# Optimization experiments

Measured on AMD Instinct MI355X. Metric: run time of the kernel, lower is better.

Reference implementation:

```python
import jax, jax.numpy as jnp
import numpy as np

N = 20000          # nodes
E = 320000         # directed edges (self-loops added in reference)
F_IN = 128         # input node features
HEADS = 8
HID = 64           # per-head hidden channels
G = 64             # graphs in the batch
NUM_CLASSES = 10
NEG_SLOPE = 0.2    # PyG GATConv LeakyReLU slope


def _gat_layer(x, src, dst, W, a_src, a_dst, bias, n_nodes):
    """PyG-style GATConv: messages flow src->dst, softmax over incoming edges."""
    H, C = a_src.shape
    h = (x @ W).reshape(n_nodes, H, C)                     # [N,H,C]
    asrc = jnp.einsum('nhc,hc->nh', h, a_src)              # [N,H]
    adst = jnp.einsum('nhc,hc->nh', h, a_dst)              # [N,H]
    e = jax.nn.leaky_relu(asrc[src] + adst[dst], NEG_SLOPE)  # [Etot,H]
    emax = jax.ops.segment_max(e, dst, num_segments=n_nodes)  # [N,H]
    ee = jnp.exp(e - emax[dst])
    denom = jax.ops.segment_sum(ee, dst, num_segments=n_nodes)
    alpha = ee / (denom[dst] + 1e-16)                      # [Etot,H]
    out = jax.ops.segment_sum(h[src] * alpha[:, :, None], dst, num_segments=n_nodes)
    return out.reshape(n_nodes, H * C) + bias


def setup_inputs() -> dict:
    key = jax.random.key(0)
    ks = jax.random.split(key, 10)
    x = jax.random.normal(ks[0], (N, F_IN), jnp.float32)
    edge_index = jax.random.randint(ks[1], (2, E), 0, N, jnp.int32)
    batch = jnp.sort(jax.random.randint(ks[2], (N,), 0, G, jnp.int32))
    # layer 1: F_IN -> HEADS*HID (concat)
    W1 = jax.random.normal(ks[3], (F_IN, HEADS * HID), jnp.float32) / np.float32(np.sqrt(F_IN))
    a_src1 = jax.random.normal(ks[4], (HEADS, HID), jnp.float32) / np.float32(np.sqrt(HID))
    a_dst1 = jax.random.normal(ks[5], (HEADS, HID), jnp.float32) / np.float32(np.sqrt(HID))
    b1 = jnp.zeros((HEADS * HID,), jnp.float32)
    # layer 2: HEADS*HID -> NUM_CLASSES (1 head)
    W2 = jax.random.normal(ks[6], (HEADS * HID, NUM_CLASSES), jnp.float32) / np.float32(np.sqrt(HEADS * HID))
    a_src2 = jax.random.normal(ks[7], (1, NUM_CLASSES), jnp.float32) / np.float32(np.sqrt(NUM_CLASSES))
    a_dst2 = jax.random.normal(ks[8], (1, NUM_CLASSES), jnp.float32) / np.float32(np.sqrt(NUM_CLASSES))
    b2 = jnp.zeros((NUM_CLASSES,), jnp.float32)
    return {"x": x, "edge_index": edge_index, "batch": batch,
            "W1": W1, "a_src1": a_src1, "a_dst1": a_dst1, "b1": b1,
            "W2": W2, "a_src2": a_src2, "a_dst2": a_dst2, "b2": b2}


def reference(x, edge_index, batch, W1, a_src1, a_dst1, b1, W2, a_src2, a_dst2, b2):
    n = x.shape[0]
    loop = jnp.arange(n, dtype=edge_index.dtype)   # add_self_loops=True (PyG default)
    src = jnp.concatenate([edge_index[0], loop])
    dst = jnp.concatenate([edge_index[1], loop])
    h = jax.nn.elu(_gat_layer(x, src, dst, W1, a_src1, a_dst1, b1, n))
    h = _gat_layer(h, src, dst, W2, a_src2, a_dst2, b2, n)
    # PowerMeanAggregation with default p=1.0 == mean pooling per graph
    sums = jax.ops.segment_sum(h, batch, num_segments=G)                    # [G,NC]
    counts = jax.ops.segment_sum(jnp.ones((n, 1), h.dtype), batch, num_segments=G)
    return sums / jnp.maximum(counts, 1.0)
```

## Files before the change

### kernel.cpp

```cpp
#include <hip/hip_runtime.h>
#include <hip/hip_bf16.h>

typedef unsigned short ushort_t;
typedef unsigned int uint_t;
typedef unsigned char uchar_t;

typedef __attribute__((ext_vector_type(8))) short bf16x8;
typedef __attribute__((ext_vector_type(4))) float f32x4;
typedef __attribute__((ext_vector_type(2))) float f32x2;

__device__ __forceinline__ float bf2f(ushort_t u) {
    union { uint_t i; float f; } v; v.i = ((uint_t)u) << 16; return v.f;
}
__device__ __forceinline__ ushort_t f2bf(float f) {
    __hip_bfloat16 h = __float2bfloat16(f);
    ushort_t u; __builtin_memcpy(&u, &h, 2); return u;
}
__device__ __forceinline__ uchar_t f2fp8(float v) {
    int p = __builtin_amdgcn_cvt_pk_fp8_f32(v, v, 0, false);
    return (uchar_t)(p & 0xff);
}
__device__ __forceinline__ float leaky(float v) { return (v > 0.f) ? v : 0.2f * v; }

#define PO_AS1 0
#define PO_AD1 512
#define PO_B1  1024
#define PO_W2  1536
#define PO_AS2 6656
#define PO_AD2 6666
#define PO_B2  6676
#define PTOT   6686

__device__ __forceinline__ bool detect_fp32_local(const ushort_t* __restrict__ xa) {
    __shared__ int cnt;
    if (threadIdx.x == 0) cnt = 0;
    __syncthreads();
    int bad = 0;
    for (int i = threadIdx.x; i < 4096; i += 256) {
        float v = bf2f(xa[i]);
        if (!(fabsf(v) < 1e4f)) bad++;
    }
    if (bad) atomicAdd(&cnt, bad);
    __syncthreads();
    return cnt >= 16;
}

__global__ __launch_bounds__(256) void k_prep(const void* __restrict__ x,
                                              const void* __restrict__ W1,
                                              const void* as1, const void* ad1,
                                              const void* b1, const void* W2,
                                              const void* as2, const void* ad2,
                                              const void* b2,
                                              ushort_t* __restrict__ W1t,
                                              float* __restrict__ prm,
                                              int* __restrict__ deg,
                                              float* __restrict__ gacc,
                                              int* __restrict__ flag, int N) {
    int b = blockIdx.x, t = threadIdx.x;
    if (b < 283) {
        bool isf = detect_fp32_local((const ushort_t*)x);
        if (b == 0 && t == 0) *flag = isf ? 1 : 0;
        if (b < 256) {
            int idx = b * 256 + t;
            int n = idx & 511, k = idx >> 9;
            float v = isf ? ((const float*)W1)[k * 512 + n]
                          : bf2f(((const ushort_t*)W1)[k * 512 + n]);
            W1t[n * 128 + k] = f2bf(v);
        } else {
            int i = (b - 256) * 256 + t;
            if (i < PTOT) {
                const void* src; int off;
                if (i < 512)       { src = as1; off = i; }
                else if (i < 1024) { src = ad1; off = i - 512; }
                else if (i < 1536) { src = b1;  off = i - 1024; }
                else if (i < 6656) { src = W2;  off = i - 1536; }
                else if (i < 6666) { src = as2; off = i - 6656; }
                else if (i < 6676) { src = ad2; off = i - 6666; }
                else               { src = b2;  off = i - 6676; }
                prm[i] = isf ? ((const float*)src)[off] : bf2f(((const ushort_t*)src)[off]);
            }
        }
    } else if (b < 362) {
        int i = (b - 283) * 256 + t;
        if (i < N) deg[i] = 0;
    } else {
        for (int i = t; i < 640; i += 256) gacc[i] = 0.f;
    }
}

__global__ __launch_bounds__(256) void k_gemm_hist(const void* __restrict__ xraw,
                                                   const ushort_t* __restrict__ w1t,
                                                   const float* __restrict__ prm,
                                                   const int* __restrict__ ei,
                                                   const int* __restrict__ flag,
                                                   uchar_t* __restrict__ h1,
                                                   float* __restrict__ asrcf,
                                                   float* __restrict__ adstf,
                                                   int* __restrict__ deg,
                                                   int E, int Etot) {
    int b = blockIdx.x, t = threadIdx.x;
    if (b >= 1250) {
        int e = (b - 1250) * 256 + t;
        if (e < Etot) {
            int dst = (e < E) ? ei[E + e] : (e - E);
            atomicAdd(&deg[dst], 1);
        }
        return;
    }
    int wave = t >> 6, lane = t & 63;
    int m0 = b * 16;
    bool isf = (*flag != 0);
    __shared__ ushort_t sA[16 * 128];
    {
        ushort_t tmp[8];
        if (isf) {
            const float4* x4 = (const float4*)((const float*)xraw + (size_t)m0 * 128);
            float4 f0 = x4[2 * t], f1 = x4[2 * t + 1];
            tmp[0] = f2bf(f0.x); tmp[1] = f2bf(f0.y); tmp[2] = f2bf(f0.z); tmp[3] = f2bf(f0.w);
            tmp[4] = f2bf(f1.x); tmp[5] = f2bf(f1.y); tmp[6] = f2bf(f1.z); tmp[7] = f2bf(f1.w);
        } else {
            const uint4* x4 = (const uint4*)((const ushort_t*)xraw + (size_t)m0 * 128);
            uint4 u = x4[t];
            __builtin_memcpy(tmp, &u, 16);
        }
        *reinterpret_cast<uint4*>(&sA[t * 8]) = *reinterpret_cast<uint4*>(tmp);
    }
    __syncthreads();
    int mr = lane & 15, quad = lane >> 4;
    int n0 = wave * 128;
    f32x4 acc[8];
#pragma unroll
    for (int ct = 0; ct < 8; ++ct) acc[ct] = {0.f, 0.f, 0.f, 0.f};
#pragma unroll
    for (int kk = 0; kk < 4; ++kk) {
        bf16x8 a = *reinterpret_cast<const bf16x8*>(&sA[mr * 128 + quad * 8 + kk * 32]);
#pragma unroll
        for (int ct = 0; ct < 8; ++ct) {
            bf16x8 bb = *reinterpret_cast<const bf16x8*>(
                &w1t[(size_t)(n0 + ct * 16 + mr) * 128 + quad * 8 + kk * 32]);
            acc[ct] = __builtin_amdgcn_mfma_f32_16x16x32_bf16(a, bb, acc[ct], 0, 0, 0);
        }
    }
    int col = lane & 15;
#pragma unroll
    for (int hh = 0; hh < 2; ++hh) {
        float ps[4] = {0.f, 0.f, 0.f, 0.f}, pd[4] = {0.f, 0.f, 0.f, 0.f};
#pragma unroll
        for (int c4 = 0; c4 < 4; ++c4) {
            int ct = hh * 4 + c4;
            int abscol = n0 + ct * 16 + col;
            float asv = prm[PO_AS1 + abscol];
            float adv = prm[PO_AD1 + abscol];
#pragma unroll
            for (int r = 0; r < 4; ++r) {
                h1[(size_t)(m0 + quad * 4 + r) * 512 + abscol] = f2fp8(acc[ct][r]);
                ps[r] += acc[ct][r] * asv;
                pd[r] += acc[ct][r] * adv;
            }
        }
#pragma unroll
        for (int off = 1; off <= 8; off <<= 1) {
#pragma unroll
            for (int r = 0; r < 4; ++r) {
                ps[r] += __shfl_xor(ps[r], off, 64);
                pd[r] += __shfl_xor(pd[r], off, 64);
            }
        }
        if (col == 0) {
            int head = 2 * wave + hh;
#pragma unroll
            for (int r = 0; r < 4; ++r) {
                asrcf[(m0 + quad * 4 + r) * 8 + head] = ps[r];
                adstf[(m0 + quad * 4 + r) * 8 + head] = pd[r];
            }
        }
    }
}

__global__ __launch_bounds__(256) void k_scan(const int* __restrict__ deg,
                                              int* __restrict__ rowptr,
                                              int* __restrict__ cursor, int N) {
    int b = blockIdx.x, t = threadIdx.x;
    int lane = t & 63, wv = t >> 6;
    __shared__ int ws[4], wt[4];
    __shared__ int sbase;
    int limit = b * 256;
    int partial = 0;
    for (int i = t; i < limit; i += 256) partial += deg[i];
#pragma unroll
    for (int off = 32; off; off >>= 1) partial += __shfl_xor(partial, off, 64);
    if (lane == 0) ws[wv] = partial;
    __syncthreads();
    if (t == 0) sbase = ws[0] + ws[1] + ws[2] + ws[3];
    __syncthreads();
    int base = sbase;
    int i = limit + t;
    int v = (i < N) ? deg[i] : 0;
    int inc = v;
#pragma unroll
    for (int off = 1; off < 64; off <<= 1) {
        int u = __shfl_up(inc, off, 64);
        if (lane >= off) inc += u;
    }
    if (lane == 63) wt[wv] = inc;
    __syncthreads();
    int woff = 0;
    for (int w = 0; w < 4; ++w) if (w < wv) woff += wt[w];
    int excl = base + woff + inc - v;
    if (i < N) { rowptr[i + 1] = excl + v; cursor[i] = excl; }
    if (i == 0) rowptr[0] = 0;
}

__global__ __launch_bounds__(256) void k_scatter(const int* __restrict__ ei,
                                                 int* __restrict__ cursor,
                                                 const float* __restrict__ asrcf,
                                                 const float* __restrict__ adstf,
                                                 int* __restrict__ csr_src,
                                                 float* __restrict__ wcsr,
                                                 int E, int Etot) {
    int e = blockIdx.x * 256 + threadIdx.x;
    if (e >= Etot) return;
    int src, dst;
    if (e < E) { src = ei[e]; dst = ei[E + e]; } else { src = dst = e - E; }
    int pos = atomicAdd(&cursor[dst], 1);
    csr_src[pos] = src;
    const float4* ap = (const float4*)&asrcf[(size_t)src * 8];
    const float4* bp = (const float4*)&adstf[(size_t)dst * 8];
    float4 a0 = ap[0], a1 = ap[1];
    float4 b0 = bp[0], b1 = bp[1];
    float4 w0, w1;
    w0.x = __expf(leaky(a0.x + b0.x));
    w0.y = __expf(leaky(a0.y + b0.y));
    w0.z = __expf(leaky(a0.z + b0.z));
    w0.w = __expf(leaky(a0.w + b0.w));
    w1.x = __expf(leaky(a1.x + b1.x));
    w1.y = __expf(leaky(a1.y + b1.y));
    w1.z = __expf(leaky(a1.z + b1.z));
    w1.w = __expf(leaky(a1.w + b1.w));
    float4* wp = (float4*)&wcsr[(size_t)pos * 8];
    wp[0] = w0; wp[1] = w1;
}

__global__ __launch_bounds__(256) void k_agg1(const uchar_t* __restrict__ h1,
                                              const int* __restrict__ rowptr,
                                              const int* __restrict__ csr_src,
                                              const float* __restrict__ wcsr,
                                              const float* __restrict__ prm,
                                              float* __restrict__ h2,
                                              float* __restrict__ asrc2f,
                                              float* __restrict__ adst2f) {
    int wid = threadIdx.x >> 6;
    int ni = wid >> 1;
    int half = wid & 1;
    int n = blockIdx.x * 2 + ni;
    int lane = threadIdx.x & 63;
    int hh = lane >> 3;
    int cb = lane * 8;
    int start = rowptr[n], end = rowptr[n + 1];
    int deg = end - start;
    int mid = (deg + 1) >> 1;
    int es = start + (half ? mid : 0);
    int ee = half ? end : (start + mid);
    float a0 = 0.f, a1 = 0.f, a2 = 0.f, a3 = 0.f, a4 = 0.f, a5 = 0.f, a6 = 0.f, a7 = 0.f;
    float den = 0.f;
    for (int base = es; base < ee; base += 64) {
        int m = min(64, ee - base);
        int sIdx = csr_src[base + min(lane, m - 1)];
        for (int g = 0; g < m; g += 8) {
            int s[8]; float w[8]; uint2 p[8];
#pragma unroll
            for (int j = 0; j < 8; ++j)
                s[j] = __shfl(sIdx, min(g + j, m - 1), 64);
#pragma unroll
            for (int j = 0; j < 8; ++j)
                w[j] = wcsr[(size_t)(base + min(g + j, m - 1)) * 8 + hh];
#pragma unroll
            for (int j = 0; j < 8; ++j)
                p[j] = *reinterpret_cast<const uint2*>(&h1[(size_t)s[j] * 512 + cb]);
#pragma unroll
            for (int j = 0; j < 8; ++j) {
                float we = (g + j < m) ? w[j] : 0.f;
                den += we;
                f32x2 q0 = __builtin_amdgcn_cvt_pk_f32_fp8((int)p[j].x, false);
                f32x2 q1 = __builtin_amdgcn_cvt_pk_f32_fp8((int)p[j].x, true);
                f32x2 q2 = __builtin_amdgcn_cvt_pk_f32_fp8((int)p[j].y, false);
                f32x2 q3 = __builtin_amdgcn_cvt_pk_f32_fp8((int)p[j].y, true);
                a0 += we * q0.x; a1 += we * q0.y;
                a2 += we * q1.x; a3 += we * q1.y;
                a4 += we * q2.x; a5 += we * q2.y;
                a6 += we * q3.x; a7 += we * q3.y;
            }
        }
    }
    __shared__ float sred[2][64][9];
    if (half) {
        float* sp = sred[ni][lane];
        sp[0] = a0; sp[1] = a1; sp[2] = a2; sp[3] = a3;
        sp[4] = a4; sp[5] = a5; sp[6] = a6; sp[7] = a7; sp[8] = den;
    }
    __syncthreads();
    if (half) return;
    {
        const float* sp = sred[ni][lane];
        a0 += sp[0]; a1 += sp[1]; a2 += sp[2]; a3 += sp[3];
        a4 += sp[4]; a5 += sp[5]; a6 += sp[6]; a7 += sp[7]; den += sp[8];
    }
    float inv = 1.f / (den + 1e-16f);
    float r[8] = {a0, a1, a2, a3, a4, a5, a6, a7};
    float p2[10];
#pragma unroll
    for (int c = 0; c < 10; ++c) p2[c] = 0.f;
#pragma unroll
    for (int j = 0; j < 8; ++j) {
        float rv = r[j] * inv + prm[PO_B1 + cb + j];
        rv = (rv > 0.f) ? rv : expm1f(rv);
#pragma unroll
        for (int c = 0; c < 10; ++c)
            p2[c] += rv * prm[PO_W2 + (cb + j) * 10 + c];
    }
#pragma unroll
    for (int c = 0; c < 10; ++c)
#pragma unroll
        for (int off = 32; off; off >>= 1)
            p2[c] += __shfl_xor(p2[c], off, 64);
    if (lane == 0) {
        float as = 0.f, ad = 0.f;
#pragma unroll
        for (int c = 0; c < 10; ++c) {
            h2[(size_t)n * 16 + c] = p2[c];
            as += p2[c] * prm[PO_AS2 + c];
            ad += p2[c] * prm[PO_AD2 + c];
        }
        asrc2f[n] = as; adst2f[n] = ad;
    }
}

__global__ __launch_bounds__(256) void k_agg2(const float* __restrict__ h2,
                                              const float* __restrict__ asrc2f,
                                              const float* __restrict__ adst2f,
                                              const int* __restrict__ rowptr,
                                              const int* __restrict__ csr_src,
                                              const float* __restrict__ prm,
                                              const int* __restrict__ batch,
                                              float* __restrict__ gacc) {
    int t = threadIdx.x;
    int grp = t >> 4, l = t & 15;
    int n = blockIdx.x * 16 + grp;
    int start = rowptr[n], end = rowptr[n + 1];
    float adn = adst2f[n];
    float den = 0.f;
    float oc[10];
#pragma unroll
    for (int c = 0; c < 10; ++c) oc[c] = 0.f;
    for (int e = start + l; e < end; e += 16) {
        int s = csr_src[e];
        float lo = asrc2f[s];
        const float4* hp = reinterpret_cast<const float4*>(&h2[(size_t)s * 16]);
        float4 q0 = hp[0], q1 = hp[1];
        float2 q2 = *reinterpret_cast<const float2*>(&h2[(size_t)s * 16 + 8]);
        float ee = __expf(leaky(lo + adn));
        den += ee;
        oc[0] += ee * q0.x; oc[1] += ee * q0.y; oc[2] += ee * q0.z; oc[3] += ee * q0.w;
        oc[4] += ee * q1.x; oc[5] += ee * q1.y; oc[6] += ee * q1.z; oc[7] += ee * q1.w;
        oc[8] += ee * q2.x; oc[9] += ee * q2.y;
    }
#pragma unroll
    for (int off = 8; off; off >>= 1) {
        den += __shfl_xor(den, off, 64);
#pragma unroll
        for (int c = 0; c < 10; ++c) oc[c] += __shfl_xor(oc[c], off, 64);
    }
    __shared__ float sres[16][11];
    __shared__ int sg[16];
    if (l == 0) {
        float invd = 1.f / (den + 1e-16f);
#pragma unroll
        for (int c = 0; c < 10; ++c) sres[grp][c] = oc[c] * invd + prm[PO_B2 + c];
        sg[grp] = batch[n];
    }
    __syncthreads();
    if (t < 10) {
        int c = t;
        float run = sres[0][c]; int g = sg[0];
        for (int k = 1; k < 16; ++k) {
            if (sg[k] != g) {
                atomicAdd(&gacc[g * 10 + c], run);
                g = sg[k]; run = 0.f;
            }
            run += sres[k][c];
        }
        atomicAdd(&gacc[g * 10 + c], run);
    }
}

__global__ void k_final(const float* __restrict__ gacc,
                        const int* __restrict__ batch,
                        const int* __restrict__ flag,
                        void* __restrict__ dout, int N) {
    int g = threadIdx.x;
    if (g >= 64) return;
    bool isf = (*flag != 0);
    int lo = 0, hi = N;
    while (lo < hi) { int mid = (lo + hi) >> 1; if (batch[mid] < g) lo = mid + 1; else hi = mid; }
    int lo2 = lo, hi2 = N;
    while (lo2 < hi2) { int mid = (lo2 + hi2) >> 1; if (batch[mid] < g + 1) lo2 = mid + 1; else hi2 = mid; }
    int count = lo2 - lo;
    float cnt = (float)(count > 0 ? count : 1);
    for (int c = 0; c < 10; ++c) {
        float r = gacc[g * 10 + c] / cnt;
        if (isf) ((float*)dout)[g * 10 + c] = r;
        else     ((ushort_t*)dout)[g * 10 + c] = f2bf(r);
    }
}

extern "C" void kernel_launch(void* const* d_in, const int* in_sizes, int n_in,
                              void* d_out, int out_size, void* d_ws, size_t ws_size,
                              hipStream_t stream) {
    const void* x   = d_in[0];
    const int* ei   = (const int*)d_in[1];
    const int* batch= (const int*)d_in[2];
    const void* W1  = d_in[3];
    const void* as1 = d_in[4];
    const void* ad1 = d_in[5];
    const void* b1  = d_in[6];
    const void* W2  = d_in[7];
    const void* as2 = d_in[8];
    const void* ad2 = d_in[9];
    const void* b2  = d_in[10];

    constexpr int N = 20000, E = 320000, Etot = E + N;
    constexpr int histBlocks = (Etot + 255) / 256;

    char* p = (char*)d_ws;
    auto alloc = [&](size_t bytes) {
        char* r = p; p += (bytes + 255) & ~(size_t)255; return r;
    };
    int* flag       = (int*)alloc(256);
    float* prm      = (float*)alloc((size_t)PTOT * 4);
    ushort_t* w1t   = (ushort_t*)alloc(512 * 128 * 2);
    uchar_t* h1     = (uchar_t*)alloc((size_t)N * 512);
    float* asrc1f   = (float*)alloc((size_t)N * 8 * 4);
    float* adst1f   = (float*)alloc((size_t)N * 8 * 4);
    float* asrc2f   = (float*)alloc((size_t)N * 4);
    float* adst2f   = (float*)alloc((size_t)N * 4);
    float* h2       = (float*)alloc((size_t)N * 16 * 4);
    float* gacc     = (float*)alloc((size_t)64 * 10 * 4);
    int* deg        = (int*)alloc((size_t)N * 4);
    int* rowptr     = (int*)alloc((size_t)(N + 1) * 4);
    int* cursor     = (int*)alloc((size_t)N * 4);
    int* csr_src    = (int*)alloc((size_t)Etot * 4);
    float* wcsr     = (float*)alloc((size_t)Etot * 8 * 4);

    k_prep<<<363, 256, 0, stream>>>(x, W1, as1, ad1, b1, W2, as2, ad2, b2,
                                    w1t, prm, deg, gacc, flag, N);
    k_gemm_hist<<<1250 + histBlocks, 256, 0, stream>>>(x, w1t, prm, ei, flag, h1,
                                                       asrc1f, adst1f, deg, E, Etot);
    k_scan<<<(N + 255) / 256, 256, 0, stream>>>(deg, rowptr, cursor, N);
    k_scatter<<<histBlocks, 256, 0, stream>>>(ei, cursor, asrc1f, adst1f,
                                              csr_src, wcsr, E, Etot);
    k_agg1<<<N / 2, 256, 0, stream>>>(h1, rowptr, csr_src, wcsr, prm,
                                      h2, asrc2f, adst2f);
    k_agg2<<<N / 16, 256, 0, stream>>>(h2, asrc2f, adst2f, rowptr, csr_src, prm,
                                       batch, gacc);
    k_final<<<1, 64, 0, stream>>>(gacc, batch, flag, d_out, N);
}
```

Measured before the change: 241.1 us.

## Compute edge attention weights inside aggregation and accumulate graph counts via atomics

Drops the per-edge precomputed weight array (wcsr, 8 floats per edge) from the scatter kernel. The aggregation kernel now recomputes exp(leaky(asrc[src]+adst[dst])) on the fly from the per-node attention scalars. This removes a large write plus read of edge-weight memory at the cost of extra exp work and a gathered asrc load per edge. It also counts nodes per graph with atomics in agg2, replacing the binary search in k_final, and vectorizes the W2 row loads.

```diff
diff --git a/kernel.cpp b/kernel.cpp
--- a/kernel.cpp
+++ b/kernel.cpp
@@ -84,7 +84,7 @@
         int i = (b - 283) * 256 + t;
         if (i < N) deg[i] = 0;
     } else {
-        for (int i = t; i < 640; i += 256) gacc[i] = 0.f;
+        for (int i = t; i < 704; i += 256) gacc[i] = 0.f;
     }
 }
 
@@ -213,10 +213,7 @@
 
 __global__ __launch_bounds__(256) void k_scatter(const int* __restrict__ ei,
                                                  int* __restrict__ cursor,
-                                                 const float* __restrict__ asrcf,
-                                                 const float* __restrict__ adstf,
                                                  int* __restrict__ csr_src,
-                                                 float* __restrict__ wcsr,
                                                  int E, int Etot) {
     int e = blockIdx.x * 256 + threadIdx.x;
     if (e >= Etot) return;
@@ -224,27 +221,13 @@
     if (e < E) { src = ei[e]; dst = ei[E + e]; } else { src = dst = e - E; }
     int pos = atomicAdd(&cursor[dst], 1);
     csr_src[pos] = src;
-    const float4* ap = (const float4*)&asrcf[(size_t)src * 8];
-    const float4* bp = (const float4*)&adstf[(size_t)dst * 8];
-    float4 a0 = ap[0], a1 = ap[1];
-    float4 b0 = bp[0], b1 = bp[1];
-    float4 w0, w1;
-    w0.x = __expf(leaky(a0.x + b0.x));
-    w0.y = __expf(leaky(a0.y + b0.y));
-    w0.z = __expf(leaky(a0.z + b0.z));
-    w0.w = __expf(leaky(a0.w + b0.w));
-    w1.x = __expf(leaky(a1.x + b1.x));
-    w1.y = __expf(leaky(a1.y + b1.y));
-    w1.z = __expf(leaky(a1.z + b1.z));
-    w1.w = __expf(leaky(a1.w + b1.w));
-    float4* wp = (float4*)&wcsr[(size_t)pos * 8];
-    wp[0] = w0; wp[1] = w1;
 }
 
 __global__ __launch_bounds__(256) void k_agg1(const uchar_t* __restrict__ h1,
+                                              const float* __restrict__ asrcf,
+                                              const float* __restrict__ adstf,
                                               const int* __restrict__ rowptr,
                                               const int* __restrict__ csr_src,
-                                              const float* __restrict__ wcsr,
                                               const float* __restrict__ prm,
                                               float* __restrict__ h2,
                                               float* __restrict__ asrc2f,
@@ -261,25 +244,26 @@
     int mid = (deg + 1) >> 1;
     int es = start + (half ? mid : 0);
     int ee = half ? end : (start + mid);
+    float adh = adstf[n * 8 + hh];
     float a0 = 0.f, a1 = 0.f, a2 = 0.f, a3 = 0.f, a4 = 0.f, a5 = 0.f, a6 = 0.f, a7 = 0.f;
     float den = 0.f;
     for (int base = es; base < ee; base += 64) {
         int m = min(64, ee - base);
         int sIdx = csr_src[base + min(lane, m - 1)];
         for (int g = 0; g < m; g += 8) {
-            int s[8]; float w[8]; uint2 p[8];
+            int s[8]; float lo[8]; uint2 p[8];
 #pragma unroll
             for (int j = 0; j < 8; ++j)
                 s[j] = __shfl(sIdx, min(g + j, m - 1), 64);
 #pragma unroll
             for (int j = 0; j < 8; ++j)
-                w[j] = wcsr[(size_t)(base + min(g + j, m - 1)) * 8 + hh];
+                lo[j] = asrcf[s[j] * 8 + hh];
 #pragma unroll
             for (int j = 0; j < 8; ++j)
                 p[j] = *reinterpret_cast<const uint2*>(&h1[(size_t)s[j] * 512 + cb]);
 #pragma unroll
             for (int j = 0; j < 8; ++j) {
-                float we = (g + j < m) ? w[j] : 0.f;
+                float we = (g + j < m) ? __expf(leaky(lo[j] + adh)) : 0.f;
                 den += we;
                 f32x2 q0 = __builtin_amdgcn_cvt_pk_f32_fp8((int)p[j].x, false);
                 f32x2 q1 = __builtin_amdgcn_cvt_pk_f32_fp8((int)p[j].x, true);
@@ -314,9 +298,13 @@
     for (int j = 0; j < 8; ++j) {
         float rv = r[j] * inv + prm[PO_B1 + cb + j];
         rv = (rv > 0.f) ? rv : expm1f(rv);
-#pragma unroll
-        for (int c = 0; c < 10; ++c)
-            p2[c] += rv * prm[PO_W2 + (cb + j) * 10 + c];
+        const float2* wrow = reinterpret_cast<const float2*>(&prm[PO_W2 + (cb + j) * 10]);
+        float2 w01 = wrow[0], w23 = wrow[1], w45 = wrow[2], w67 = wrow[3], w89 = wrow[4];
+        p2[0] += rv * w01.x; p2[1] += rv * w01.y;
+        p2[2] += rv * w23.x; p2[3] += rv * w23.y;
+        p2[4] += rv * w45.x; p2[5] += rv * w45.y;
+        p2[6] += rv * w67.x; p2[7] += rv * w67.y;
+        p2[8] += rv * w89.x; p2[9] += rv * w89.y;
     }
 #pragma unroll
     for (int c = 0; c < 10; ++c)
@@ -342,7 +330,8 @@
                                               const int* __restrict__ csr_src,
                                               const float* __restrict__ prm,
                                               const int* __restrict__ batch,
-                                              float* __restrict__ gacc) {
+                                              float* __restrict__ gacc,
+                                              float* __restrict__ gcnt) {
     int t = threadIdx.x;
     int grp = t >> 4, l = t & 15;
     int n = blockIdx.x * 16 + grp;
@@ -370,42 +359,38 @@
 #pragma unroll
         for (int c = 0; c < 10; ++c) oc[c] += __shfl_xor(oc[c], off, 64);
     }
-    __shared__ float sres[16][11];
+    __shared__ float sres[16][12];
     __shared__ int sg[16];
     if (l == 0) {
         float invd = 1.f / (den + 1e-16f);
 #pragma unroll
         for (int c = 0; c < 10; ++c) sres[grp][c] = oc[c] * invd + prm[PO_B2 + c];
+        sres[grp][10] = 1.f;
         sg[grp] = batch[n];
     }
     __syncthreads();
-    if (t < 10) {
+    if (t < 11) {
         int c = t;
         float run = sres[0][c]; int g = sg[0];
         for (int k = 1; k < 16; ++k) {
             if (sg[k] != g) {
-                atomicAdd(&gacc[g * 10 + c], run);
+                atomicAdd(c < 10 ? &gacc[g * 10 + c] : &gcnt[g], run);
                 g = sg[k]; run = 0.f;
             }
             run += sres[k][c];
         }
-        atomicAdd(&gacc[g * 10 + c], run);
+        atomicAdd(c < 10 ? &gacc[g * 10 + c] : &gcnt[g], run);
     }
 }
 
 __global__ void k_final(const float* __restrict__ gacc,
-                        const int* __restrict__ batch,
+                        const float* __restrict__ gcnt,
                         const int* __restrict__ flag,
-                        void* __restrict__ dout, int N) {
+                        void* __restrict__ dout) {
     int g = threadIdx.x;
     if (g >= 64) return;
     bool isf = (*flag != 0);
-    int lo = 0, hi = N;
-    while (lo < hi) { int mid = (lo + hi) >> 1; if (batch[mid] < g) lo = mid + 1; else hi = mid; }
-    int lo2 = lo, hi2 = N;
-    while (lo2 < hi2) { int mid = (lo2 + hi2) >> 1; if (batch[mid] < g + 1) lo2 = mid + 1; else hi2 = mid; }
-    int count = lo2 - lo;
-    float cnt = (float)(count > 0 ? count : 1);
+    float cnt = fmaxf(gcnt[g], 1.f);
     for (int c = 0; c < 10; ++c) {
         float r = gacc[g * 10 + c] / cnt;
         if (isf) ((float*)dout)[g * 10 + c] = r;
@@ -444,23 +429,22 @@
     float* asrc2f   = (float*)alloc((size_t)N * 4);
     float* adst2f   = (float*)alloc((size_t)N * 4);
     float* h2       = (float*)alloc((size_t)N * 16 * 4);
-    float* gacc     = (float*)alloc((size_t)64 * 10 * 4);
+    float* gacc     = (float*)alloc((size_t)(64 * 10 + 64) * 4);
     int* deg        = (int*)alloc((size_t)N * 4);
     int* rowptr     = (int*)alloc((size_t)(N + 1) * 4);
     int* cursor     = (int*)alloc((size_t)N * 4);
-    int* csr_src    = (int*)alloc((size_t)Etot * 4);
-    float* wcsr     = (float*)alloc((size_t)Etot * 8 * 4);
+    int* csr_src    = (int*)alloc((size_t)(Etot + 64) * 4);
+    float* gcnt     = gacc + 640;
 
     k_prep<<<363, 256, 0, stream>>>(x, W1, as1, ad1, b1, W2, as2, ad2, b2,
                                     w1t, prm, deg, gacc, flag, N);
     k_gemm_hist<<<1250 + histBlocks, 256, 0, stream>>>(x, w1t, prm, ei, flag, h1,
                                                        asrc1f, adst1f, deg, E, Etot);
     k_scan<<<(N + 255) / 256, 256, 0, stream>>>(deg, rowptr, cursor, N);
-    k_scatter<<<histBlocks, 256, 0, stream>>>(ei, cursor, asrc1f, adst1f,
-                                              csr_src, wcsr, E, Etot);
-    k_agg1<<<N / 2, 256, 0, stream>>>(h1, rowptr, csr_src, wcsr, prm,
+    k_scatter<<<histBlocks, 256, 0, stream>>>(ei, cursor, csr_src, E, Etot);
+    k_agg1<<<N / 2, 256, 0, stream>>>(h1, asrc1f, adst1f, rowptr, csr_src, prm,
                                       h2, asrc2f, adst2f);
     k_agg2<<<N / 16, 256, 0, stream>>>(h2, asrc2f, adst2f, rowptr, csr_src, prm,
-                                       batch, gacc);
-    k_final<<<1, 64, 0, stream>>>(gacc, batch, flag, d_out, N);
-}
+                                       batch, gacc, gcnt);
+    k_final<<<1, 64, 0, stream>>>(gacc, gcnt, flag, d_out);
+}
```

Result: no change. 245.5 us (+1.8%).
